# Performance work log

Measured on AMD Instinct MI355X. Metric: run time of the kernel, lower is better.

Reference implementation:

```python
import jax, jax.numpy as jnp
import numpy as np
from jax import lax

KS, STRIDE, DIL, PAD = 3, 1, 1, 1
B, C_IN, C_OUT, D = 1, 16, 16, 64
K = KS ** 3


def setup_inputs():
    key = jax.random.key(0)
    k1, k2, k3 = jax.random.split(key, 3)
    x = jax.random.normal(k1, (B, C_IN, D, D, D), jnp.float32)
    std = 1.0 / float(np.sqrt(C_IN * K))
    kernel = jax.random.uniform(k2, (K, C_IN, C_OUT), jnp.float32, -std, std)
    # module zero-inits pkernel; use small random values so interp path is exercised
    pkernel = jax.random.normal(k3, (K, C_IN, 3 * K), jnp.float32) * 0.01
    return {"x": x, "kernel": kernel, "pkernel": pkernel}


def _deform_conv3d(x, kernel, pkernel):
    Bn, C, Dd, H, W = x.shape
    Kt = kernel.shape[0]
    # offset-predicting conv: pkernel [K, C_in, 3K] -> conv weight [3K, C_in, kd, kh, kw]
    w_off = jnp.transpose(pkernel.reshape(KS, KS, KS, C, 3 * Kt), (4, 3, 0, 1, 2))
    off = lax.conv_general_dilated(
        x, w_off, (STRIDE,) * 3, [(PAD, PAD)] * 3,
        rhs_dilation=(DIL,) * 3,
        dimension_numbers=("NCDHW", "OIDHW", "NCDHW"))
    Do, Ho, Wo = off.shape[2], off.shape[3], off.shape[4]
    off = off.reshape(Bn, Kt, 3, Do, Ho, Wo)  # 3 offset coords per kernel tap

    # base sampling grid: out_pos*stride - pad + tap*dilation, then add predicted offset
    r = jnp.arange(KS)
    tap = jnp.stack(jnp.meshgrid(r, r, r, indexing="ij"), -1).reshape(Kt, 3) * DIL - PAD
    gz = (jnp.arange(Do) * STRIDE).astype(x.dtype)
    gy = (jnp.arange(Ho) * STRIDE).astype(x.dtype)
    gx = (jnp.arange(Wo) * STRIDE).astype(x.dtype)
    cz = gz[None, None, :, None, None] + tap[None, :, 0, None, None, None] + off[:, :, 0]
    cy = gy[None, None, None, :, None] + tap[None, :, 1, None, None, None] + off[:, :, 1]
    cx = gx[None, None, None, None, :] + tap[None, :, 2, None, None, None] + off[:, :, 2]

    x_flat = x.reshape(Bn, C, Dd * H * W)

    def gather(idx):  # idx [B,K,Do,Ho,Wo] int32 -> [B,C,K,Do,Ho,Wo]
        g = jax.vmap(lambda xf, ix: xf[:, ix.reshape(-1)])(x_flat, idx)
        return g.reshape(Bn, C, Kt, Do, Ho, Wo)

    z0f = jnp.floor(cz); y0f = jnp.floor(cy); x0f = jnp.floor(cx)
    fz, fy, fx = cz - z0f, cy - y0f, cx - x0f
    z0 = z0f.astype(jnp.int32); y0 = y0f.astype(jnp.int32); x0 = x0f.astype(jnp.int32)

    # trilinear interp: accumulate 8 corners (zero outside volume)
    acc = jnp.zeros((Bn, C, Kt, Do, Ho, Wo), x.dtype)
    for dz in (0, 1):
        for dy in (0, 1):
            for dx in (0, 1):
                zi, yi, xi = z0 + dz, y0 + dy, x0 + dx
                valid = ((zi >= 0) & (zi < Dd) & (yi >= 0) & (yi < H)
                         & (xi >= 0) & (xi < W)).astype(x.dtype)
                w = ((fz if dz else 1.0 - fz) * (fy if dy else 1.0 - fy)
                     * (fx if dx else 1.0 - fx)) * valid
                idx = (jnp.clip(zi, 0, Dd - 1) * (H * W)
                       + jnp.clip(yi, 0, H - 1) * W + jnp.clip(xi, 0, W - 1))
                acc = acc + gather(idx) * w[:, None]

    # weighted sum over taps: kernel [K, C_in, C_out]
    return jnp.einsum("bckdhw,kco->bodhw", acc, kernel)


def reference(x, kernel, pkernel):
    return _deform_conv3d(x, kernel, pkernel)
```

## Files before the change

### kernel.cpp

```cpp
#include <hip/hip_runtime.h>

#define D 64
#define DD 4096
#define DDD 262144
#define K 27

typedef _Float16 half8  __attribute__((ext_vector_type(8)));
typedef _Float16 half4v __attribute__((ext_vector_type(4)));
typedef _Float16 half2v __attribute__((ext_vector_type(2)));
typedef float    f32x4  __attribute__((ext_vector_type(4)));
typedef float    f32x2  __attribute__((ext_vector_type(2)));

__device__ inline half2v pk2(float w) {
    return __builtin_bit_cast(half2v, __builtin_amdgcn_cvt_pkrtz(w, w));
}
__device__ inline half2v h2of(half8 v, int d) {
    half2v r; r.x = v[2*d]; r.y = v[2*d+1]; return r;
}

#define HX 12
#define HY 8
#define HZ 6
#define HROW 12
#define HPLN 96
#define HSP  576
#define AS   4608

#define WSW_CH (14*6*64)
#define KSW_CH (14*64)
#define KSW_OFF 86016
#define TAPF_OFF (KSW_OFF + KSW_CH*16)

__device__ constexpr int dispf(int k) {
    int kk = (k < K) ? k : 0;
    return ((kk / 9) + 1) * HPLN + (((kk / 3) % 3) + 1) * HROW + ((kk % 3) + 1);
}

__global__ __launch_bounds__(256) void prep_weights(const float* __restrict__ pk,
                                                    const float* __restrict__ kern,
                                                    _Float16* __restrict__ Wsw,
                                                    _Float16* __restrict__ Ksw,
                                                    float* __restrict__ tapf) {
    int t = blockIdx.x * 256 + threadIdx.x;
    if (t < WSW_CH) {
        int lane = t & 63;
        int sm = t >> 6;
        int s = sm / 6, mt = sm - 6 * s;
        int m = mt * 16 + (lane & 15);
        int q = lane >> 4;
        half8 w;
#pragma unroll
        for (int j = 0; j < 8; ++j) {
            int k = 32 * s + 8 * q + j;
            int kt = k >> 4, c = k & 15;
            float wv = (kt < K && m < 81) ? pk[kt * 1296 + c * 81 + m] : 0.0f;
            w[j] = (_Float16)wv;
        }
        *(half8*)(Wsw + t * 8) = w;
    } else if (t < WSW_CH + KSW_CH) {
        int u = t - WSW_CH;
        int lane = u & 63;
        int cch = u >> 6;
        int s = cch >> 1, h = cch & 1;
        int o = lane & 15;
        int tap = 4 * s + (lane >> 4);
        half8 w;
#pragma unroll
        for (int j = 0; j < 8; ++j) {
            int ch = h * 8 + j;
            float wv = (tap < K) ? kern[tap * 256 + ch * 16 + o] : 0.0f;
            w[j] = (_Float16)wv;
        }
        *(half8*)(Ksw + u * 8) = w;
    } else if (t < WSW_CH + KSW_CH + 28) {
        int kt = t - WSW_CH - KSW_CH;
        int ktc = (kt < K) ? kt : K - 1;
        int kd = ktc / 9, kh = (ktc / 3) % 3, kw = ktc % 3;
        f32x4 b;
        b.x = (float)(kd + 1);
        b.y = (float)(kh + 1);
        b.z = (float)(kw + 1);
        b.w = 0.0f;
        *(f32x4*)(tapf + kt * 4) = b;
    }
}

__global__ __launch_bounds__(256, 4) void deform_main(
    const float* __restrict__ x,
    const _Float16* __restrict__ Wsw,
    const _Float16* __restrict__ Ksw,
    const float* __restrict__ tapf,
    float* __restrict__ out)
{
    __shared__ _Float16 s_h[2 * AS];
    __shared__ _Float16 s_off[K * 64 * 4];

    const int tid  = threadIdx.x;
    const int lane = tid & 63;
    const int wave = __builtin_amdgcn_readfirstlane(tid >> 6);

    const int bx0 = blockIdx.x * 8;
    const int by0 = blockIdx.y * 4;
    const int bz0 = blockIdx.z * 2;

    for (int i = tid; i < HSP; i += 256) {
        int z = i / HPLN;
        int r = i - z * HPLN;
        int y = r / HROW;
        int xx = r - y * HROW;
        int gz = bz0 - 2 + z, gy = by0 - 2 + y, gx = bx0 - 2 + xx;
        bool in = (unsigned)gz < D && (unsigned)gy < D && (unsigned)gx < D;
        half8 a = {}, b = {};
        if (in) {
            const float* p = x + (gz * DD + gy * D + gx);
#pragma unroll
            for (int c = 0; c < 8; ++c) a[c] = (_Float16)p[c * DDD];
#pragma unroll
            for (int c = 0; c < 8; ++c) b[c] = (_Float16)p[(c + 8) * DDD];
        }
        *(half8*)(s_h + i * 8)      = a;
        *(half8*)(s_h + AS + i * 8) = b;
    }
    __syncthreads();

    const int n = lane & 15, q = lane >> 4;
    const int tz = wave >> 1;
    const int ty = 2 * (wave & 1) + (n >> 3);
    const int tx = n & 7;
    const int v = wave * 16 + n;

    {
        const int qh = q >> 1;
        const int vbase = tz * HPLN + ty * HROW + tx;
        const _Float16* hbase = s_h + (q & 1) * AS;
        f32x4 acc[6] = {};

        half8 bfr, afr[6];
        bfr = *(const half8*)(hbase + (vbase + (qh ? dispf(1) : dispf(0))) * 8);
#pragma unroll
        for (int mt = 0; mt < 6; ++mt)
            afr[mt] = *(const half8*)(Wsw + (mt * 64 + lane) * 8);

#pragma unroll
        for (int s = 0; s < 14; ++s) {
            half8 bnx, anx[6];
            if (s < 13) {
                int disp = qh ? dispf(2 * (s + 1) + 1) : dispf(2 * (s + 1));
                bnx = *(const half8*)(hbase + (vbase + disp) * 8);
#pragma unroll
                for (int mt = 0; mt < 6; ++mt)
                    anx[mt] = *(const half8*)(Wsw + (((s + 1) * 6 + mt) * 64 + lane) * 8);
            }
#pragma unroll
            for (int mt = 0; mt < 6; ++mt)
                acc[mt] = __builtin_amdgcn_mfma_f32_16x16x32_f16(afr[mt], bfr, acc[mt], 0, 0, 0);
            bfr = bnx;
#pragma unroll
            for (int mt = 0; mt < 6; ++mt) afr[mt] = anx[mt];
        }

#pragma unroll
        for (int mt = 0; mt < 6; ++mt)
#pragma unroll
            for (int r = 0; r < 4; ++r) {
                int o = mt * 16 + q * 4 + r;
                if (o < 81) {
                    int kt = (o * 171) >> 9;
                    int c = o - kt * 3;
                    s_off[kt * 256 + v * 4 + c] = (_Float16)acc[mt][r];
                }
            }
    }
    __syncthreads();

    const float bzf = (float)tz, byf = (float)ty, bxf = (float)tx;
    f32x4 acc2 = {};

    float lzv[7], lyv[7], lxv[7];
    int cb[7];
    unsigned badbits = 0;
#pragma unroll
    for (int s = 0; s < 7; ++s) {
        const int ktr = 4 * s + q;
        const int kt = (ktr < K) ? ktr : K - 1;
        const f32x4 tb = *(const f32x4*)(tapf + kt * 4);
        const half4v off3 = *(const half4v*)(s_off + kt * 256 + v * 4);
        float lz = bzf + tb.x + (float)off3[0];
        float ly = byf + tb.y + (float)off3[1];
        float lx = bxf + tb.z + (float)off3[2];
        lzv[s] = lz; lyv[s] = ly; lxv[s] = lx;
        int hz0 = (int)floorf(lz), hy0 = (int)floorf(ly), hx0 = (int)floorf(lx);
        int hz0c = min(max(hz0, 0), HZ - 2);
        int hy0c = min(max(hy0, 0), HY - 2);
        int hx0c = min(max(hx0, 0), HX - 2);
        bool mis = (hz0 != hz0c) || (hy0 != hy0c) || (hx0 != hx0c);
        badbits |= (__ballot(mis) != 0ull) ? (1u << s) : 0u;
        cb[s] = (hz0c * HPLN + hy0c * HROW + hx0c) * 8;
    }

    half8 alo = *(const half8*)(Ksw + (0 * 64 + lane) * 8);
    half8 ahi = *(const half8*)(Ksw + (1 * 64 + lane) * 8);

#pragma unroll
    for (int s = 0; s < 7; ++s) {
        half8 alo_n, ahi_n;
        if (s < 6) {
            alo_n = *(const half8*)(Ksw + ((2 * s + 2) * 64 + lane) * 8);
            ahi_n = *(const half8*)(Ksw + ((2 * s + 3) * 64 + lane) * 8);
        }

        const float lz = lzv[s], ly = lyv[s], lx = lxv[s];
        const float fz = lz - floorf(lz), fy = ly - floorf(ly), fx = lx - floorf(lx);

        half2v val2[8];
        {
            const _Float16* cpl = s_h + cb[s];
            float gz1 = 1.0f - fz, gy1 = 1.0f - fy, gx1 = 1.0f - fx;
            float wyx00 = gy1 * gx1, wyx01 = gy1 * fx;
            float wyx10 = fy * gx1,  wyx11 = fy * fx;
#pragma unroll
            for (int dz = 0; dz < 2; ++dz) {
                float wz = dz ? fz : gz1;
                const _Float16* cz_ = cpl + dz * (HPLN * 8);
                half2v h00 = pk2(wz * wyx00);
                half2v h01 = pk2(wz * wyx01);
                half2v h10 = pk2(wz * wyx10);
                half2v h11 = pk2(wz * wyx11);
                half8 l00 = *(const half8*)(cz_);
                half8 l01 = *(const half8*)(cz_ + 8);
                half8 l10 = *(const half8*)(cz_ + HROW * 8);
                half8 l11 = *(const half8*)(cz_ + (HROW + 1) * 8);
                half8 u00 = *(const half8*)(cz_ + AS);
                half8 u01 = *(const half8*)(cz_ + AS + 8);
                half8 u10 = *(const half8*)(cz_ + AS + HROW * 8);
                half8 u11 = *(const half8*)(cz_ + AS + (HROW + 1) * 8);
                if (dz == 0) {
#pragma unroll
                    for (int d = 0; d < 4; ++d) {
                        val2[d]      = h00 * h2of(l00, d);
                        val2[4 + d]  = h00 * h2of(u00, d);
                        val2[d]     += h01 * h2of(l01, d);
                        val2[4 + d] += h01 * h2of(u01, d);
                        val2[d]     += h10 * h2of(l10, d);
                        val2[4 + d] += h10 * h2of(u10, d);
                        val2[d]     += h11 * h2of(l11, d);
                        val2[4 + d] += h11 * h2of(u11, d);
                    }
                } else {
#pragma unroll
                    for (int d = 0; d < 4; ++d) {
                        val2[d]     += h00 * h2of(l00, d);
                        val2[4 + d] += h00 * h2of(u00, d);
                        val2[d]     += h01 * h2of(l01, d);
                        val2[4 + d] += h01 * h2of(u01, d);
                        val2[d]     += h10 * h2of(l10, d);
                        val2[4 + d] += h10 * h2of(u10, d);
                        val2[d]     += h11 * h2of(l11, d);
                        val2[4 + d] += h11 * h2of(u11, d);
                    }
                }
            }
        }

        if (__builtin_expect((badbits >> s) & 1u, 0)) {
            int hz0 = (int)floorf(lz), hy0 = (int)floorf(ly), hx0 = (int)floorf(lx);
            bool mis = (hz0 < 0) || (hz0 > HZ - 2) || (hy0 < 0) || (hy0 > HY - 2)
                     || (hx0 < 0) || (hx0 > HX - 2);
            if (mis) {
                int z0 = hz0 + bz0 - 2, y0 = hy0 + by0 - 2, x0 = hx0 + bx0 - 2;
                f32x2 valf[8] = {};
#pragma unroll
                for (int dz = 0; dz < 2; ++dz) {
                    int zi = z0 + dz;
                    float wz = dz ? fz : 1.0f - fz;
#pragma unroll
                    for (int dy = 0; dy < 2; ++dy) {
                        int yi = y0 + dy;
                        float wzy = wz * (dy ? fy : 1.0f - fy);
#pragma unroll
                        for (int dx = 0; dx < 2; ++dx) {
                            int xi = x0 + dx;
                            if ((unsigned)zi < D && (unsigned)yi < D && (unsigned)xi < D) {
                                float w = wzy * (dx ? fx : 1.0f - fx);
                                int base = zi * DD + yi * D + xi;
#pragma unroll
                                for (int d = 0; d < 8; ++d) {
                                    valf[d].x += w * x[(2 * d)     * DDD + base];
                                    valf[d].y += w * x[(2 * d + 1) * DDD + base];
                                }
                            }
                        }
                    }
                }
#pragma unroll
                for (int d = 0; d < 8; ++d) {
                    val2[d].x = (_Float16)valf[d].x;
                    val2[d].y = (_Float16)valf[d].y;
                }
            }
        }

        half8 blo, bhi;
#pragma unroll
        for (int d = 0; d < 4; ++d) {
            blo[2*d] = val2[d].x;     blo[2*d+1] = val2[d].y;
            bhi[2*d] = val2[4+d].x;   bhi[2*d+1] = val2[4+d].y;
        }
        acc2 = __builtin_amdgcn_mfma_f32_16x16x32_f16(alo, blo, acc2, 0, 0, 0);
        acc2 = __builtin_amdgcn_mfma_f32_16x16x32_f16(ahi, bhi, acc2, 0, 0, 0);
        alo = alo_n;
        ahi = ahi_n;
    }

    const int gz = bz0 + tz, gy = by0 + ty, gx = bx0 + tx;
    const int opos = gz * DD + gy * D + gx;
#pragma unroll
    for (int r = 0; r < 4; ++r) {
        int o = q * 4 + r;
        out[o * DDD + opos] = acc2[r];
    }
}

extern "C" void kernel_launch(void* const* d_in, const int* in_sizes, int n_in,
                              void* d_out, int out_size, void* d_ws, size_t ws_size,
                              hipStream_t stream) {
    const float* x    = (const float*)d_in[0];
    const float* kern = (const float*)d_in[1];
    const float* pk   = (const float*)d_in[2];
    float* out = (float*)d_out;

    _Float16* Wsw = (_Float16*)d_ws;
    _Float16* Ksw = (_Float16*)((char*)d_ws + KSW_OFF);
    float* tapf   = (float*)((char*)d_ws + TAPF_OFF);

    prep_weights<<<25, 256, 0, stream>>>(pk, kern, Wsw, Ksw, tapf);
    deform_main<<<dim3(8, 16, 32), 256, 0, stream>>>(x, Wsw, Ksw, tapf, out);
}
```

Measured before the change: 144.3 us.

## Remap offset-conv MFMA output so offsets land directly in registers

Reorders the offset-conv weight rows so each 16-row MFMA tile holds 4 taps by 4 coordinate slots, matching the lane/tap layout used by the sampling stage. This removes the shared-memory offset staging buffer, its fp16 round trip and a block barrier, and keeps offsets in fp32 registers. In exchange it issues 7 M-tiles instead of 6 (padding waste), and raises the launch-bounds occupancy target to 6, which may force register spills.

After: 210.9 us. 46.2% more time.

```diff
diff --git a/kernel.cpp b/kernel.cpp
--- a/kernel.cpp
+++ b/kernel.cpp
@@ -26,9 +26,9 @@
 #define HSP  576
 #define AS   4608
 
-#define WSW_CH (14*6*64)
+#define WSW_CH (14*7*64)
 #define KSW_CH (14*64)
-#define KSW_OFF 86016
+#define KSW_OFF 100352
 #define TAPF_OFF (KSW_OFF + KSW_CH*16)
 
 __device__ constexpr int dispf(int k) {
@@ -45,15 +45,18 @@
     if (t < WSW_CH) {
         int lane = t & 63;
         int sm = t >> 6;
-        int s = sm / 6, mt = sm - 6 * s;
-        int m = mt * 16 + (lane & 15);
-        int q = lane >> 4;
+        int ks = sm / 7, mt = sm - 7 * ks;
+        int m16 = lane & 15;
+        int kq = lane >> 4;
+        int kt = 4 * mt + (m16 >> 2);
+        int c  = m16 & 3;
         half8 w;
 #pragma unroll
         for (int j = 0; j < 8; ++j) {
-            int k = 32 * s + 8 * q + j;
-            int kt = k >> 4, c = k & 15;
-            float wv = (kt < K && m < 81) ? pk[kt * 1296 + c * 81 + m] : 0.0f;
+            int k = 32 * ks + 8 * kq + j;
+            int ktw = k >> 4, cin = k & 15;
+            float wv = (c < 3 && kt < K && ktw < K) ? pk[ktw * 1296 + cin * 81 + (3 * kt + c)]
+                                                    : 0.0f;
             w[j] = (_Float16)wv;
         }
         *(half8*)(Wsw + t * 8) = w;
@@ -85,7 +88,7 @@
     }
 }
 
-__global__ __launch_bounds__(256, 4) void deform_main(
+__global__ __launch_bounds__(256, 6) void deform_main(
     const float* __restrict__ x,
     const _Float16* __restrict__ Wsw,
     const _Float16* __restrict__ Ksw,
@@ -93,7 +96,6 @@
     float* __restrict__ out)
 {
     __shared__ _Float16 s_h[2 * AS];
-    __shared__ _Float16 s_off[K * 64 * 4];
 
     const int tid  = threadIdx.x;
     const int lane = tid & 63;
@@ -127,55 +129,39 @@
     const int tz = wave >> 1;
     const int ty = 2 * (wave & 1) + (n >> 3);
     const int tx = n & 7;
-    const int v = wave * 16 + n;
-
+
+    f32x4 acc1[7] = {};
     {
         const int qh = q >> 1;
         const int vbase = tz * HPLN + ty * HROW + tx;
         const _Float16* hbase = s_h + (q & 1) * AS;
-        f32x4 acc[6] = {};
-
-        half8 bfr, afr[6];
-        bfr = *(const half8*)(hbase + (vbase + (qh ? dispf(1) : dispf(0))) * 8);
-#pragma unroll
-        for (int mt = 0; mt < 6; ++mt)
+
+        half8 bfr = *(const half8*)(hbase + (vbase + (qh ? dispf(1) : dispf(0))) * 8);
+        half8 afr[7];
+#pragma unroll
+        for (int mt = 0; mt < 7; ++mt)
             afr[mt] = *(const half8*)(Wsw + (mt * 64 + lane) * 8);
 
 #pragma unroll
         for (int s = 0; s < 14; ++s) {
-            half8 bnx, anx[6];
+            half8 bnx;
             if (s < 13) {
                 int disp = qh ? dispf(2 * (s + 1) + 1) : dispf(2 * (s + 1));
                 bnx = *(const half8*)(hbase + (vbase + disp) * 8);
-#pragma unroll
-                for (int mt = 0; mt < 6; ++mt)
-                    anx[mt] = *(const half8*)(Wsw + (((s + 1) * 6 + mt) * 64 + lane) * 8);
             }
 #pragma unroll
-            for (int mt = 0; mt < 6; ++mt)
-                acc[mt] = __builtin_amdgcn_mfma_f32_16x16x32_f16(afr[mt], bfr, acc[mt], 0, 0, 0);
+            for (int mt = 0; mt < 7; ++mt) {
+                half8 anx;
+                if (s < 13)
+                    anx = *(const half8*)(Wsw + (((s + 1) * 7 + mt) * 64 + lane) * 8);
+                acc1[mt] = __builtin_amdgcn_mfma_f32_16x16x32_f16(afr[mt], bfr, acc1[mt], 0, 0, 0);
+                afr[mt] = anx;
+            }
             bfr = bnx;
-#pragma unroll
-            for (int mt = 0; mt < 6; ++mt) afr[mt] = anx[mt];
-        }
-
-#pragma unroll
-        for (int mt = 0; mt < 6; ++mt)
-#pragma unroll
-            for (int r = 0; r < 4; ++r) {
-                int o = mt * 16 + q * 4 + r;
-                if (o < 81) {
-                    int kt = (o * 171) >> 9;
-                    int c = o - kt * 3;
-                    s_off[kt * 256 + v * 4 + c] = (_Float16)acc[mt][r];
-                }
-            }
-    }
-    __syncthreads();
+        }
+    }
 
     const float bzf = (float)tz, byf = (float)ty, bxf = (float)tx;
-    f32x4 acc2 = {};
-
     float lzv[7], lyv[7], lxv[7];
     int cb[7];
     unsigned badbits = 0;
@@ -184,10 +170,9 @@
         const int ktr = 4 * s + q;
         const int kt = (ktr < K) ? ktr : K - 1;
         const f32x4 tb = *(const f32x4*)(tapf + kt * 4);
-        const half4v off3 = *(const half4v*)(s_off + kt * 256 + v * 4);
-        float lz = bzf + tb.x + (float)off3[0];
-        float ly = byf + tb.y + (float)off3[1];
-        float lx = bxf + tb.z + (float)off3[2];
+        float lz = bzf + tb.x + acc1[s][0];
+        float ly = byf + tb.y + acc1[s][1];
+        float lx = bxf + tb.z + acc1[s][2];
         lzv[s] = lz; lyv[s] = ly; lxv[s] = lx;
         int hz0 = (int)floorf(lz), hy0 = (int)floorf(ly), hx0 = (int)floorf(lx);
         int hz0c = min(max(hz0, 0), HZ - 2);
@@ -198,6 +183,7 @@
         cb[s] = (hz0c * HPLN + hy0c * HROW + hx0c) * 8;
     }
 
+    f32x4 acc2 = {};
     half8 alo = *(const half8*)(Ksw + (0 * 64 + lane) * 8);
     half8 ahi = *(const half8*)(Ksw + (1 * 64 + lane) * 8);
 
@@ -333,6 +319,6 @@
     _Float16* Ksw = (_Float16*)((char*)d_ws + KSW_OFF);
     float* tapf   = (float*)((char*)d_ws + TAPF_OFF);
 
-    prep_weights<<<25, 256, 0, stream>>>(pk, kern, Wsw, Ksw, tapf);
+    prep_weights<<<29, 256, 0, stream>>>(pk, kern, Wsw, Ksw, tapf);
     deform_main<<<dim3(8, 16, 32), 256, 0, stream>>>(x, Wsw, Ksw, tapf, out);
 }
```

## Software-pipeline LDS corner loads across taps and lower occupancy target

Applied to the files above, without the earlier changes.

Restructures the per-tap trilinear interpolation loop so the eight lower-plane corner vectors for the next tap are prefetched from LDS while the current tap is computed. The upper-plane loads are issued early in each iteration. The Ksw weight fragments are now loaded just before the MFMAs instead of being double-buffered. Launch bounds drop from 4 to 3 waves per EU to free registers for the extra prefetch buffers, which lowers occupancy and may expose latency.

After: 150.4 us. 1.04x slower.

```diff
diff --git a/kernel.cpp b/kernel.cpp
--- a/kernel.cpp
+++ b/kernel.cpp
@@ -34,6 +34,12 @@
 __device__ constexpr int dispf(int k) {
     int kk = (k < K) ? k : 0;
     return ((kk / 9) + 1) * HPLN + (((kk / 3) % 3) + 1) * HROW + ((kk % 3) + 1);
+}
+
+__device__ constexpr int coff(int c) {
+    int base = (c & 4) ? AS : 0;
+    int yx = c & 3;
+    return base + (yx >> 1) * (HROW * 8) + (yx & 1) * 8;
 }
 
 __global__ __launch_bounds__(256) void prep_weights(const float* __restrict__ pk,
@@ -85,7 +91,7 @@
     }
 }
 
-__global__ __launch_bounds__(256, 4) void deform_main(
+__global__ __launch_bounds__(256, 3) void deform_main(
     const float* __restrict__ x,
     const _Float16* __restrict__ Wsw,
     const _Float16* __restrict__ Ksw,
@@ -198,67 +204,62 @@
         cb[s] = (hz0c * HPLN + hy0c * HROW + hx0c) * 8;
     }
 
-    half8 alo = *(const half8*)(Ksw + (0 * 64 + lane) * 8);
-    half8 ahi = *(const half8*)(Ksw + (1 * 64 + lane) * 8);
+    half8 p0[8], p1[8], p0n[8];
+#pragma unroll
+    for (int c = 0; c < 8; ++c) p0[c] = *(const half8*)(s_h + cb[0] + coff(c));
 
 #pragma unroll
     for (int s = 0; s < 7; ++s) {
-        half8 alo_n, ahi_n;
-        if (s < 6) {
-            alo_n = *(const half8*)(Ksw + ((2 * s + 2) * 64 + lane) * 8);
-            ahi_n = *(const half8*)(Ksw + ((2 * s + 3) * 64 + lane) * 8);
-        }
-
         const float lz = lzv[s], ly = lyv[s], lx = lxv[s];
         const float fz = lz - floorf(lz), fy = ly - floorf(ly), fx = lx - floorf(lx);
+        const float gz1 = 1.0f - fz, gy1 = 1.0f - fy, gx1 = 1.0f - fx;
+        const float wyx00 = gy1 * gx1, wyx01 = gy1 * fx;
+        const float wyx10 = fy * gx1,  wyx11 = fy * fx;
+
+#pragma unroll
+        for (int c = 0; c < 8; ++c)
+            p1[c] = *(const half8*)(s_h + cb[s] + HPLN * 8 + coff(c));
 
         half2v val2[8];
         {
-            const _Float16* cpl = s_h + cb[s];
-            float gz1 = 1.0f - fz, gy1 = 1.0f - fy, gx1 = 1.0f - fx;
-            float wyx00 = gy1 * gx1, wyx01 = gy1 * fx;
-            float wyx10 = fy * gx1,  wyx11 = fy * fx;
-#pragma unroll
-            for (int dz = 0; dz < 2; ++dz) {
-                float wz = dz ? fz : gz1;
-                const _Float16* cz_ = cpl + dz * (HPLN * 8);
-                half2v h00 = pk2(wz * wyx00);
-                half2v h01 = pk2(wz * wyx01);
-                half2v h10 = pk2(wz * wyx10);
-                half2v h11 = pk2(wz * wyx11);
-                half8 l00 = *(const half8*)(cz_);
-                half8 l01 = *(const half8*)(cz_ + 8);
-                half8 l10 = *(const half8*)(cz_ + HROW * 8);
-                half8 l11 = *(const half8*)(cz_ + (HROW + 1) * 8);
-                half8 u00 = *(const half8*)(cz_ + AS);
-                half8 u01 = *(const half8*)(cz_ + AS + 8);
-                half8 u10 = *(const half8*)(cz_ + AS + HROW * 8);
-                half8 u11 = *(const half8*)(cz_ + AS + (HROW + 1) * 8);
-                if (dz == 0) {
-#pragma unroll
-                    for (int d = 0; d < 4; ++d) {
-                        val2[d]      = h00 * h2of(l00, d);
-                        val2[4 + d]  = h00 * h2of(u00, d);
-                        val2[d]     += h01 * h2of(l01, d);
-                        val2[4 + d] += h01 * h2of(u01, d);
-                        val2[d]     += h10 * h2of(l10, d);
-                        val2[4 + d] += h10 * h2of(u10, d);
-                        val2[d]     += h11 * h2of(l11, d);
-                        val2[4 + d] += h11 * h2of(u11, d);
-                    }
-                } else {
-#pragma unroll
-                    for (int d = 0; d < 4; ++d) {
-                        val2[d]     += h00 * h2of(l00, d);
-                        val2[4 + d] += h00 * h2of(u00, d);
-                        val2[d]     += h01 * h2of(l01, d);
-                        val2[4 + d] += h01 * h2of(u01, d);
-                        val2[d]     += h10 * h2of(l10, d);
-                        val2[4 + d] += h10 * h2of(u10, d);
-                        val2[d]     += h11 * h2of(l11, d);
-                        val2[4 + d] += h11 * h2of(u11, d);
-                    }
-                }
+            half2v h00 = pk2(gz1 * wyx00);
+            half2v h01 = pk2(gz1 * wyx01);
+            half2v h10 = pk2(gz1 * wyx10);
+            half2v h11 = pk2(gz1 * wyx11);
+#pragma unroll
+            for (int d = 0; d < 4; ++d) {
+                val2[d]      = h00 * h2of(p0[0], d);
+                val2[4 + d]  = h00 * h2of(p0[4], d);
+                val2[d]     += h01 * h2of(p0[1], d);
+                val2[4 + d] += h01 * h2of(p0[5], d);
+                val2[d]     += h10 * h2of(p0[2], d);
+                val2[4 + d] += h10 * h2of(p0[6], d);
+                val2[d]     += h11 * h2of(p0[3], d);
+                val2[4 + d] += h11 * h2of(p0[7], d);
+            }
+        }
+
+        if (s < 6) {
+#pragma unroll
+            for (int c = 0; c < 8; ++c)
+                p0n[c] = *(const half8*)(s_h + cb[s + 1] + coff(c));
+        }
+
+        {
+            half2v h00 = pk2(fz * wyx00);
+            half2v h01 = pk2(fz * wyx01);
+            half2v h10 = pk2(fz * wyx10);
+            half2v h11 = pk2(fz * wyx11);
+#pragma unroll
+            for (int d = 0; d < 4; ++d) {
+                val2[d]     += h00 * h2of(p1[0], d);
+                val2[4 + d] += h00 * h2of(p1[4], d);
+                val2[d]     += h01 * h2of(p1[1], d);
+                val2[4 + d] += h01 * h2of(p1[5], d);
+                val2[d]     += h10 * h2of(p1[2], d);
+                val2[4 + d] += h10 * h2of(p1[6], d);
+                val2[d]     += h11 * h2of(p1[3], d);
+                val2[4 + d] += h11 * h2of(p1[7], d);
             }
         }
 
@@ -306,10 +307,13 @@
             blo[2*d] = val2[d].x;     blo[2*d+1] = val2[d].y;
             bhi[2*d] = val2[4+d].x;   bhi[2*d+1] = val2[4+d].y;
         }
+        half8 alo = *(const half8*)(Ksw + ((2 * s)     * 64 + lane) * 8);
+        half8 ahi = *(const half8*)(Ksw + ((2 * s + 1) * 64 + lane) * 8);
         acc2 = __builtin_amdgcn_mfma_f32_16x16x32_f16(alo, blo, acc2, 0, 0, 0);
         acc2 = __builtin_amdgcn_mfma_f32_16x16x32_f16(ahi, bhi, acc2, 0, 0, 0);
-        alo = alo_n;
-        ahi = ahi_n;
+
+#pragma unroll
+        for (int c = 0; c < 8; ++c) p0[c] = p0n[c];
     }
 
     const int gz = bz0 + tz, gy = by0 + ty, gx = bx0 + tx;
```
